# Kernel optimization log

Measured on AMD Instinct MI355X. Metric: run time of the kernel, lower is better.

## Reference

```python
import jax, jax.numpy as jnp
import numpy as np

NEG = -9e15
ALPHA = 0.2  # leaky-relu slope


def gat_layer(h, mask, W, a, concat):
    # h: [N, Fin], W: [Fin, Fout], a: [2*Fout, 1], mask: [N, N]
    Wh = h @ W                                   # [N, Fout]
    F = Wh.shape[1]
    e = jax.nn.leaky_relu(Wh @ a[:F] + (Wh @ a[F:]).T, ALPHA)  # [N, N]
    att = jax.nn.softmax(jnp.where(mask > 0, e, NEG), axis=1)
    out = att @ Wh                               # [N, Fout]
    return jax.nn.elu(out) if concat else out


def gat(x, mask, W, a, Wo, ao):
    # W: [H, Fin, Fhid], a: [H, 2*Fhid, 1]
    heads = jax.vmap(lambda Wi, ai: gat_layer(x, mask, Wi, ai, True))(W, a)  # [H, N, Fhid]
    h = jnp.transpose(heads, (1, 0, 2)).reshape(x.shape[0], -1)  # [N, H*Fhid] (concat dim=1)
    return jax.nn.elu(gat_layer(h, mask, Wo, ao, False))


def setup_inputs() -> dict:
    key = jax.random.key(0)
    ks = jax.random.split(key, 16)
    N, Fin, H, Fhid, Ffin, P = 4096, 256, 4, 64, 64, 16
    x = jax.random.normal(ks[0], (N, Fin), jnp.float32)
    eye = jnp.eye(N, dtype=jnp.float32)
    sadj = jnp.maximum((jax.random.uniform(ks[1], (N, N)) < 0.005).astype(jnp.float32), eye)
    sadj2 = jnp.maximum((jax.random.uniform(ks[2], (N, N)) < 0.005).astype(jnp.float32), eye)
    s = 0.1
    inp = {
        "x": x, "sadj": sadj, "sadj2": sadj2,
        "W1": s * jax.random.normal(ks[3], (H, Fin, Fhid), jnp.float32),
        "a1": s * jax.random.normal(ks[4], (H, 2 * Fhid, 1), jnp.float32),
        "Wo1": s * jax.random.normal(ks[5], (H * Fhid, Ffin), jnp.float32),
        "ao1": s * jax.random.normal(ks[6], (2 * Ffin, 1), jnp.float32),
        "W2": s * jax.random.normal(ks[7], (H, Fin, Fhid), jnp.float32),
        "a2": s * jax.random.normal(ks[8], (H, 2 * Fhid, 1), jnp.float32),
        "Wo2": s * jax.random.normal(ks[9], (H * Fhid, Ffin), jnp.float32),
        "ao2": s * jax.random.normal(ks[10], (2 * Ffin, 1), jnp.float32),
        "Wp1": s * jax.random.normal(ks[11], (Ffin, P), jnp.float32),
        "bp1": jnp.zeros((P,), jnp.float32),
        "Wp2": s * jax.random.normal(ks[12], (P, 1), jnp.float32),
    }
    return inp


def reference(x, sadj, sadj2, W1, a1, Wo1, ao1, W2, a2, Wo2, ao2, Wp1, bp1, Wp2):
    emb1 = gat(x, sadj, W1, a1, Wo1, ao1)    # [N, Ffin]
    emb2 = gat(x, sadj2, W2, a2, Wo2, ao2)   # [N, Ffin]
    emb = jnp.stack([emb1, emb2], axis=1)    # [N, 2, Ffin]
    w = jnp.tanh(emb @ Wp1 + bp1) @ Wp2      # [N, 2, 1]
    beta = jax.nn.softmax(w, axis=1)
    return jnp.sum(beta * emb, axis=1)       # [N, Ffin]
```

## Files before the change

### kernel.cpp

```cpp
#include <hip/hip_runtime.h>
#include <hip/hip_bf16.h>
#include <stdint.h>


typedef short short8 __attribute__((ext_vector_type(8)));
typedef __bf16 bf16x8 __attribute__((ext_vector_type(8)));
typedef float floatx4 __attribute__((ext_vector_type(4)));
typedef unsigned int uintx4 __attribute__((ext_vector_type(4)));

#define MAXDEG 128
#define LRELU 0.2f

template <typename V>
__device__ inline auto mfma_impl(V a, V b, floatx4 c, int)
    -> decltype(__builtin_amdgcn_mfma_f32_16x16x32_bf16(a, b, c, 0, 0, 0)) {
  return __builtin_amdgcn_mfma_f32_16x16x32_bf16(a, b, c, 0, 0, 0);
}
template <typename V>
__device__ inline floatx4 mfma_impl(V a, V b, floatx4 c, long) {
  return __builtin_amdgcn_mfma_f32_16x16x32_bf16(
      __builtin_bit_cast(bf16x8, a), __builtin_bit_cast(bf16x8, b), c, 0, 0, 0);
}
__device__ inline floatx4 MFMA16(short8 a, short8 b, floatx4 c) {
  return mfma_impl(a, b, c, 0);
}

__device__ inline bool is_bf16_inputs(const void* sadj) {
  return ((*(const uint32_t*)sadj) & 0xFFFFu) == 0x3F80u;
}
__device__ inline float ldval(const void* p, size_t i, bool isbf) {
  if (isbf) return __bfloat162float(((const __hip_bfloat16*)p)[i]);
  return ((const float*)p)[i];
}
__device__ inline uint16_t f2bf_bits(float f) {
  __hip_bfloat16 h = __float2bfloat16(f);
  return *(uint16_t*)&h;
}
__device__ inline float bf2f(uint16_t u) {
  uint32_t i = ((uint32_t)u) << 16;
  return __builtin_bit_cast(float, i);
}

static constexpr size_t OFF_ADJ = 0;
static constexpr size_t OFF_DEG = OFF_ADJ + (size_t)2 * 4096 * MAXDEG * 4;
static constexpr size_t OFF_XB  = OFF_DEG + (size_t)2 * 4096 * 4;
static constexpr size_t OFF_WT  = OFF_XB  + (size_t)4096 * 256 * 2;
static constexpr size_t OFF_WOT = OFF_WT  + (size_t)2 * 4 * 64 * 256 * 2;
static constexpr size_t OFF_AV  = OFF_WOT + (size_t)2 * 64 * 256 * 2;
static constexpr size_t OFF_AOV = OFF_AV  + (size_t)2 * 4 * 128 * 4;
static constexpr size_t OFF_WP1 = OFF_AOV + (size_t)2 * 128 * 4;
static constexpr size_t OFF_BP1 = OFF_WP1 + (size_t)64 * 16 * 4;
static constexpr size_t OFF_WP2 = OFF_BP1 + 64;
static constexpr size_t OFF_WH1B = OFF_WP2 + 192;
static constexpr size_t OFF_S1  = OFF_WH1B + (size_t)2 * 4096 * 256 * 2;
static constexpr size_t OFF_D1  = OFF_S1  + (size_t)2 * 4 * 4096 * 4;
static constexpr size_t OFF_H2  = OFF_D1  + (size_t)2 * 4 * 4096 * 4;
static constexpr size_t OFF_WH2B = OFF_H2 + (size_t)2 * 4096 * 256 * 2;
static constexpr size_t OFF_S2  = OFF_WH2B + (size_t)2 * 4096 * 64 * 2;
static constexpr size_t OFF_D2  = OFF_S2  + (size_t)2 * 4096 * 4;
static constexpr size_t OFF_MB  = OFF_D2  + (size_t)2 * 4096 * 4;

__global__ __launch_bounds__(256) void k_pre(const void* sadj, const void* sadj2,
    const void* x,
    const void* W1, const void* W2, const void* Wo1, const void* Wo2,
    const void* a1, const void* a2, const void* ao1, const void* ao2,
    const void* wp1, const void* bp1, const void* wp2,
    uint8_t* mbytes, uint16_t* xb, uint16_t* Wt, uint16_t* Wot,
    float* Av, float* Aov, float* Wp1v, float* Bp1v, float* Wp2v) {
  bool isbf = is_bf16_inputs(sadj);
  int bid = blockIdx.x;
  if (bid < 2048) {
    int tid = bid * 256 + threadIdx.x;
    int nt = 2048 * 256;
    const int NCHUNK = 4194304;
    if (isbf) {
      const uint16_t* m0 = (const uint16_t*)sadj;
      const uint16_t* m1 = (const uint16_t*)sadj2;
      for (int c = tid; c < NCHUNK; c += nt) {
        const uint16_t* src = (c < 2097152) ? m0 : m1;
        int cc = c & 2097151;
        uintx4 v = *((const uintx4*)src + cc);
        uint32_t wd[4] = {v.x, v.y, v.z, v.w};
        uint32_t byte = 0;
#pragma unroll
        for (int k = 0; k < 8; ++k) {
          uint16_t val = (uint16_t)(wd[k >> 1] >> ((k & 1) * 16));
          if (val != 0 && !(val & 0x8000)) byte |= 1u << k;
        }
        mbytes[c] = (uint8_t)byte;
      }
    } else {
      const float* m0 = (const float*)sadj;
      const float* m1 = (const float*)sadj2;
      for (int c = tid; c < NCHUNK; c += nt) {
        const float* src = (c < 2097152) ? m0 : m1;
        size_t cc = (size_t)(c & 2097151) * 8;
        floatx4 va = *(const floatx4*)(src + cc);
        floatx4 vb = *(const floatx4*)(src + cc + 4);
        float vals[8] = {va.x, va.y, va.z, va.w, vb.x, vb.y, vb.z, vb.w};
        uint32_t byte = 0;
#pragma unroll
        for (int k = 0; k < 8; ++k)
          if (vals[k] > 0.f) byte |= 1u << k;
        mbytes[c] = (uint8_t)byte;
      }
    }
    return;
  }
  if (bid < 3072) {
    int i0 = ((bid - 2048) * 256 + threadIdx.x) * 4;
    if (isbf) {
      *(uint64_t*)(xb + i0) = *(const uint64_t*)((const uint16_t*)x + i0);
    } else {
      const float* xf = (const float*)x;
      float4 f = *(const float4*)(xf + i0);
      xb[i0 + 0] = f2bf_bits(f.x);
      xb[i0 + 1] = f2bf_bits(f.y);
      xb[i0 + 2] = f2bf_bits(f.z);
      xb[i0 + 3] = f2bf_bits(f.w);
    }
    return;
  }
  int idx = (bid - 3072) * 256 + threadIdx.x;
  if (idx < 131072) {
    int k = idx & 255, f = (idx >> 8) & 63, h = (idx >> 14) & 3, g = idx >> 16;
    const void* W = g ? W2 : W1;
    Wt[idx] = f2bf_bits(ldval(W, (size_t)h * 16384 + (size_t)k * 64 + f, isbf));
  } else if (idx < 163840) {
    int j = idx - 131072;
    int k = j & 255, f = (j >> 8) & 63, g = j >> 14;
    const void* W = g ? Wo2 : Wo1;
    Wot[j] = f2bf_bits(ldval(W, (size_t)k * 64 + f, isbf));
  } else if (idx < 166176) {
    int q = idx - 163840;
    if (q < 512)        Av[q] = ldval(a1, q, isbf);
    else if (q < 1024)  Av[q] = ldval(a2, q - 512, isbf);
    else if (q < 1152)  Aov[q - 1024] = ldval(ao1, q - 1024, isbf);
    else if (q < 1280)  Aov[q - 1152 + 128] = ldval(ao2, q - 1152, isbf);
    else if (q < 2304)  Wp1v[q - 1280] = ldval(wp1, q - 1280, isbf);
    else if (q < 2320)  Bp1v[q - 2304] = ldval(bp1, q - 2304, isbf);
    else                Wp2v[q - 2320] = ldval(wp2, q - 2320, isbf);
  }
}

__global__ __launch_bounds__(256) void k_cg(const uint8_t* mbytes,
    const uint16_t* xb, const uint16_t* Wt, const float* Av,
    int* adj, int* deg, uint16_t* Wh1b, float* s1, float* d1) {
  int bid = blockIdx.x;
  if (bid < 2048) {
    int w = bid * 4 + (threadIdx.x >> 6);
    int lane = threadIdx.x & 63;
    uint64_t bits = *((const uint64_t*)(mbytes + (size_t)w * 512) + lane);
    int* out = adj + (size_t)w * MAXDEG;
    int c = __popcll(bits);
    int pre = c;
#pragma unroll
    for (int o = 1; o < 64; o <<= 1) {
      int tv = __shfl_up(pre, o);
      if (lane >= o) pre += tv;
    }
    int total = __shfl(pre, 63);
    int off = pre - c;
    int base = lane * 64;
    while (bits) {
      int i = __ffsll((unsigned long long)bits) - 1;
      bits &= bits - 1;
      if (off < MAXDEG) out[off] = base + i;
      ++off;
    }
    if (lane == 0) deg[w] = total < MAXDEG ? total : MAXDEG;
    return;
  }
  int w = (bid - 2048) * 4 + (threadIdx.x >> 6);
  int lane = threadIdx.x & 63;
  int q = lane >> 4, c = lane & 15;
  int g = w >> 10, rem = w & 1023;
  int m0 = (rem >> 2) << 4, h = rem & 3;
  const uint16_t* B = Wt + (size_t)(g * 4 + h) * 64 * 256;
  floatx4 acc[4] = {};
  const uint16_t* arow = xb + (size_t)(m0 + c) * 256 + q * 8;
  for (int kk = 0; kk < 8; ++kk) {
    short8 a = *(const short8*)(arow + kk * 32);
#pragma unroll
    for (int t = 0; t < 4; ++t) {
      short8 b = *(const short8*)(B + (size_t)(t * 16 + c) * 256 + kk * 32 + q * 8);
      acc[t] = MFMA16(a, b, acc[t]);
    }
  }
  uint16_t* Crow = Wh1b + (size_t)(g * 4096 + m0) * 256 + h * 64;
#pragma unroll
  for (int t = 0; t < 4; ++t)
#pragma unroll
    for (int r = 0; r < 4; ++r)
      Crow[(size_t)(q * 4 + r) * 256 + t * 16 + c] = f2bf_bits(acc[t][r]);
  const float* ag = Av + (g * 4 + h) * 128;
  float as[4], ad[4];
#pragma unroll
  for (int t = 0; t < 4; ++t) { as[t] = ag[t * 16 + c]; ad[t] = ag[64 + t * 16 + c]; }
#pragma unroll
  for (int r = 0; r < 4; ++r) {
    float ps = 0.f, pd = 0.f;
#pragma unroll
    for (int t = 0; t < 4; ++t) { ps += acc[t][r] * as[t]; pd += acc[t][r] * ad[t]; }
#pragma unroll
    for (int o = 1; o < 16; o <<= 1) { ps += __shfl_xor(ps, o); pd += __shfl_xor(pd, o); }
    if (c == 0) {
      int n = m0 + q * 4 + r;
      s1[((size_t)(g * 4096 + n)) * 4 + h] = ps;
      d1[((size_t)(g * 4096 + n)) * 4 + h] = pd;
    }
  }
}

__global__ __launch_bounds__(256) void k_att1(const int* adj, const int* deg,
    const float* s1, const float* d1, const uint16_t* Wh1b, uint16_t* h2) {
  __shared__ float pbuf[4][4][MAXDEG];
  __shared__ int jbuf[4][MAXDEG];
  int wv = threadIdx.x >> 6, lane = threadIdx.x & 63;
  int w = blockIdx.x * 4 + wv;
  int g = w >> 12;
  int gn = w;
  int dg = deg[gn];
  const int* nbr = adj + (size_t)gn * MAXDEG;
  float4 s4 = *(const float4*)(s1 + (size_t)gn * 4);
  const float4* d4 = (const float4*)(d1) + (size_t)g * 4096;

  bool v0 = lane < dg, v1 = lane + 64 < dg;
  int j0 = 0, j1 = 0;
  if (v0) j0 = nbr[lane];
  if (v1) j1 = nbr[lane + 64];
  float4 dj0 = d4[j0];
  float4 dj1 = d4[j1];
  if (v0) jbuf[wv][lane] = j0;
  if (v1) jbuf[wv][lane + 64] = j1;

  const float ninf = -3.0e38f;
  float sa[4] = {s4.x, s4.y, s4.z, s4.w};
  float d0a[4] = {dj0.x, dj0.y, dj0.z, dj0.w};
  float d1a[4] = {dj1.x, dj1.y, dj1.z, dj1.w};
#pragma unroll
  for (int h = 0; h < 4; ++h) {
    float t0 = sa[h] + d0a[h]; t0 = t0 > 0.f ? t0 : LRELU * t0;
    float t1 = sa[h] + d1a[h]; t1 = t1 > 0.f ? t1 : LRELU * t1;
    float e0 = v0 ? t0 : ninf;
    float e1 = v1 ? t1 : ninf;
    float m = fmaxf(e0, e1);
#pragma unroll
    for (int o = 32; o; o >>= 1) m = fmaxf(m, __shfl_xor(m, o));
    float p0 = v0 ? __expf(e0 - m) : 0.f;
    float p1 = v1 ? __expf(e1 - m) : 0.f;
    float l = p0 + p1;
#pragma unroll
    for (int o = 32; o; o >>= 1) l += __shfl_xor(l, o);
    float inv = __frcp_rn(l);
    pbuf[wv][h][lane] = p0 * inv;
    pbuf[wv][h][lane + 64] = p1 * inv;
  }
  int myh = lane >> 4;
  const float* prow = pbuf[wv][myh];
  const int* jb = jbuf[wv];
  const uint16_t* Wg = Wh1b + (size_t)g * 4096 * 256;
  float ax = 0.f, ay = 0.f, az = 0.f, aw = 0.f;
  for (int i = 0; i < dg; i += 8) {
    float pv[8];
    ushort4 wv8[8];
#pragma unroll
    for (int k = 0; k < 8; ++k) {
      int idx = i + k;
      bool vv = idx < dg;
      int sidx = vv ? idx : 0;
      int j = jb[sidx];
      pv[k] = vv ? prow[sidx] : 0.f;
      wv8[k] = *(const ushort4*)(Wg + (size_t)j * 256 + lane * 4);
    }
#pragma unroll
    for (int k = 0; k < 8; ++k) {
      ax += pv[k] * bf2f(wv8[k].x);
      ay += pv[k] * bf2f(wv8[k].y);
      az += pv[k] * bf2f(wv8[k].z);
      aw += pv[k] * bf2f(wv8[k].w);
    }
  }
  ax = ax > 0.f ? ax : __expf(ax) - 1.f;
  ay = ay > 0.f ? ay : __expf(ay) - 1.f;
  az = az > 0.f ? az : __expf(az) - 1.f;
  aw = aw > 0.f ? aw : __expf(aw) - 1.f;
  ushort4 o4 = {f2bf_bits(ax), f2bf_bits(ay), f2bf_bits(az), f2bf_bits(aw)};
  *(ushort4*)(h2 + (size_t)gn * 256 + lane * 4) = o4;
}

__global__ __launch_bounds__(256) void k_gemm2(const uint16_t* h2, const uint16_t* Wot,
                                               const float* Aov,
                                               uint16_t* Wh2b, float* s2, float* d2) {
  int w = blockIdx.x * 4 + (threadIdx.x >> 6);
  int lane = threadIdx.x & 63;
  int q = lane >> 4, c = lane & 15;
  int g = w >> 8, m0 = (w & 255) << 4;
  const uint16_t* A = h2 + (size_t)g * 4096 * 256;
  const uint16_t* B = Wot + (size_t)g * 64 * 256;
  floatx4 acc[4] = {};
  const uint16_t* arow = A + (size_t)(m0 + c) * 256 + q * 8;
  for (int kk = 0; kk < 8; ++kk) {
    short8 a = *(const short8*)(arow + kk * 32);
#pragma unroll
    for (int t = 0; t < 4; ++t) {
      short8 b = *(const short8*)(B + (size_t)(t * 16 + c) * 256 + kk * 32 + q * 8);
      acc[t] = MFMA16(a, b, acc[t]);
    }
  }
  uint16_t* Crow = Wh2b + (size_t)(g * 4096 + m0) * 64;
#pragma unroll
  for (int t = 0; t < 4; ++t)
#pragma unroll
    for (int r = 0; r < 4; ++r)
      Crow[(size_t)(q * 4 + r) * 64 + t * 16 + c] = f2bf_bits(acc[t][r]);
  const float* ag = Aov + g * 128;
  float as[4], ad[4];
#pragma unroll
  for (int t = 0; t < 4; ++t) { as[t] = ag[t * 16 + c]; ad[t] = ag[64 + t * 16 + c]; }
#pragma unroll
  for (int r = 0; r < 4; ++r) {
    float ps = 0.f, pd = 0.f;
#pragma unroll
    for (int t = 0; t < 4; ++t) { ps += acc[t][r] * as[t]; pd += acc[t][r] * ad[t]; }
#pragma unroll
    for (int o = 1; o < 16; o <<= 1) { ps += __shfl_xor(ps, o); pd += __shfl_xor(pd, o); }
    if (c == 0) {
      int n = m0 + q * 4 + r;
      s2[g * 4096 + n] = ps;
      d2[g * 4096 + n] = pd;
    }
  }
}

__global__ __launch_bounds__(256) void k_att2f(const int* adj, const int* deg,
    const float* s2, const float* d2, const uint16_t* Wh2b,
    const float* Wp1v, const float* Bp1v, const float* Wp2v,
    const void* sadj, void* out) {
  __shared__ float pbuf[4][MAXDEG];
  __shared__ int jbuf[4][MAXDEG];
  __shared__ float emb_s[4][64];
  __shared__ float st_s[2][32];
  __shared__ float sw_s[2][2];
  int wv = threadIdx.x >> 6, lane = threadIdx.x & 63;
  int g = wv >> 1, nl = wv & 1;
  int n = blockIdx.x * 2 + nl;
  int gn = g * 4096 + n;
  int dg = deg[gn];
  const int* nbr = adj + (size_t)gn * MAXDEG;
  float sn = s2[gn];
  const float* dp = d2 + (size_t)g * 4096;

  bool v0 = lane < dg, v1 = lane + 64 < dg;
  int j0 = 0, j1 = 0;
  if (v0) j0 = nbr[lane];
  if (v1) j1 = nbr[lane + 64];
  float dd0 = dp[j0], dd1 = dp[j1];
  if (v0) jbuf[wv][lane] = j0;
  if (v1) jbuf[wv][lane + 64] = j1;

  const float ninf = -3.0e38f;
  float t0 = sn + dd0; t0 = t0 > 0.f ? t0 : LRELU * t0;
  float t1 = sn + dd1; t1 = t1 > 0.f ? t1 : LRELU * t1;
  float e0 = v0 ? t0 : ninf;
  float e1 = v1 ? t1 : ninf;
  float m = fmaxf(e0, e1);
#pragma unroll
  for (int o = 32; o; o >>= 1) m = fmaxf(m, __shfl_xor(m, o));
  float p0 = v0 ? __expf(e0 - m) : 0.f;
  float p1 = v1 ? __expf(e1 - m) : 0.f;
  float l = p0 + p1;
#pragma unroll
  for (int o = 32; o; o >>= 1) l += __shfl_xor(l, o);
  float inv = __frcp_rn(l);
  pbuf[wv][lane] = p0 * inv;
  pbuf[wv][lane + 64] = p1 * inv;

  int mye = lane >> 4, c4 = lane & 15;
  const uint16_t* Wg = Wh2b + (size_t)g * 4096 * 64;
  float ax = 0.f, ay = 0.f, az = 0.f, aw = 0.f;
  for (int i = 0; i < dg; i += 8) {
    int ia = i + mye, ib = i + 4 + mye;
    bool va = ia < dg, vb = ib < dg;
    int sa_ = va ? ia : 0, sb_ = vb ? ib : 0;
    int ja = jbuf[wv][sa_], jb2 = jbuf[wv][sb_];
    float pa = va ? pbuf[wv][sa_] : 0.f;
    float pb = vb ? pbuf[wv][sb_] : 0.f;
    ushort4 wa = *(const ushort4*)(Wg + (size_t)ja * 64 + c4 * 4);
    ushort4 wb = *(const ushort4*)(Wg + (size_t)jb2 * 64 + c4 * 4);
    ax += pa * bf2f(wa.x) + pb * bf2f(wb.x);
    ay += pa * bf2f(wa.y) + pb * bf2f(wb.y);
    az += pa * bf2f(wa.z) + pb * bf2f(wb.z);
    aw += pa * bf2f(wa.w) + pb * bf2f(wb.w);
  }
#pragma unroll
  for (int o = 16; o <= 32; o <<= 1) {
    ax += __shfl_xor(ax, o);
    ay += __shfl_xor(ay, o);
    az += __shfl_xor(az, o);
    aw += __shfl_xor(aw, o);
  }
  if (lane < 16) {
    ax = ax > 0.f ? ax : __expf(ax) - 1.f;
    ay = ay > 0.f ? ay : __expf(ay) - 1.f;
    az = az > 0.f ? az : __expf(az) - 1.f;
    aw = aw > 0.f ? aw : __expf(aw) - 1.f;
    float4 r = {ax, ay, az, aw};
    *(float4*)&emb_s[wv][c4 * 4] = r;
  }
  __syncthreads();
  if (wv < 2) {
    float e1v = emb_s[wv][lane];
    float e2v = emb_s[2 + wv][lane];
    if (lane < 32) {
      int gg = lane >> 4, p = lane & 15;
      float s = Bp1v[p];
      const float* eb = emb_s[gg * 2 + wv];
      for (int f = 0; f < 64; ++f) s += eb[f] * Wp1v[f * 16 + p];
      st_s[wv][lane] = tanhf(s);
    }
    if (lane < 2) {
      float s = 0.f;
      for (int p = 0; p < 16; ++p) s += st_s[wv][lane * 16 + p] * Wp2v[p];
      sw_s[wv][lane] = s;
    }
    float w0 = sw_s[wv][0], w1 = sw_s[wv][1];
    float mx = fmaxf(w0, w1);
    float q0 = __expf(w0 - mx), q1 = __expf(w1 - mx);
    float qi = 1.f / (q0 + q1);
    float v = (q0 * e1v + q1 * e2v) * qi;
    if (is_bf16_inputs(sadj)) ((uint16_t*)out)[(size_t)n * 64 + lane] = f2bf_bits(v);
    else ((float*)out)[(size_t)n * 64 + lane] = v;
  }
}

extern "C" void kernel_launch(void* const* d_in, const int* in_sizes, int n_in,
                              void* d_out, int out_size, void* d_ws, size_t ws_size,
                              hipStream_t stream) {
  const void* x    = d_in[0];
  const void* sadj = d_in[1];
  const void* sadj2 = d_in[2];
  const void* W1  = d_in[3];
  const void* a1  = d_in[4];
  const void* Wo1 = d_in[5];
  const void* ao1 = d_in[6];
  const void* W2  = d_in[7];
  const void* a2  = d_in[8];
  const void* Wo2 = d_in[9];
  const void* ao2 = d_in[10];
  const void* Wp1 = d_in[11];
  const void* bp1 = d_in[12];
  const void* Wp2 = d_in[13];

  char* ws = (char*)d_ws;
  int* adj      = (int*)(ws + OFF_ADJ);
  int* deg      = (int*)(ws + OFF_DEG);
  uint16_t* xb  = (uint16_t*)(ws + OFF_XB);
  uint16_t* Wt  = (uint16_t*)(ws + OFF_WT);
  uint16_t* Wot = (uint16_t*)(ws + OFF_WOT);
  float* Av     = (float*)(ws + OFF_AV);
  float* Aov    = (float*)(ws + OFF_AOV);
  float* Wp1v   = (float*)(ws + OFF_WP1);
  float* Bp1v   = (float*)(ws + OFF_BP1);
  float* Wp2v   = (float*)(ws + OFF_WP2);
  uint16_t* Wh1b = (uint16_t*)(ws + OFF_WH1B);
  float* s1     = (float*)(ws + OFF_S1);
  float* d1     = (float*)(ws + OFF_D1);
  uint16_t* h2  = (uint16_t*)(ws + OFF_H2);
  uint16_t* Wh2b = (uint16_t*)(ws + OFF_WH2B);
  float* s2     = (float*)(ws + OFF_S2);
  float* d2     = (float*)(ws + OFF_D2);
  uint8_t* mb   = (uint8_t*)(ws + OFF_MB);

  k_pre<<<3728, 256, 0, stream>>>(sadj, sadj2, x, W1, W2, Wo1, Wo2,
                                  a1, a2, ao1, ao2, Wp1, bp1, Wp2,
                                  mb, xb, Wt, Wot, Av, Aov, Wp1v, Bp1v, Wp2v);
  k_cg<<<2560, 256, 0, stream>>>(mb, xb, Wt, Av, adj, deg, Wh1b, s1, d1);
  k_att1<<<2048, 256, 0, stream>>>(adj, deg, s1, d1, Wh1b, h2);
  k_gemm2<<<128, 256, 0, stream>>>(h2, Wot, Aov, Wh2b, s2, d2);
  k_att2f<<<2048, 256, 0, stream>>>(adj, deg, s2, d2, Wh2b,
                                    Wp1v, Bp1v, Wp2v, sadj, d_out);
}
```

Baseline: 232.1 us.

## Build adjacency lists per row directly from masks, dropping packed bitmask stage

Removes the intermediate packed mask-byte buffer. Each adjacency row is now compacted in one 256-thread block that reads the dense mask row, builds bits and does a block-wide prefix scan. The old combined pre/compaction kernel is split into separate adjacency kernels and a standalone first GEMM kernel. A device-to-device copy of the first mask into workspace is also added; it costs extra memory traffic and reserves more workspace, and the copy is only read on the bf16 path.

```diff
diff --git a/kernel.cpp b/kernel.cpp
--- a/kernel.cpp
+++ b/kernel.cpp
@@ -58,57 +58,18 @@
 static constexpr size_t OFF_WH2B = OFF_H2 + (size_t)2 * 4096 * 256 * 2;
 static constexpr size_t OFF_S2  = OFF_WH2B + (size_t)2 * 4096 * 64 * 2;
 static constexpr size_t OFF_D2  = OFF_S2  + (size_t)2 * 4096 * 4;
-static constexpr size_t OFF_MB  = OFF_D2  + (size_t)2 * 4096 * 4;
-
-__global__ __launch_bounds__(256) void k_pre(const void* sadj, const void* sadj2,
-    const void* x,
+static constexpr size_t OFF_M0  = OFF_D2  + (size_t)2 * 4096 * 4;
+
+__global__ __launch_bounds__(256) void k_pre(const void* x,
     const void* W1, const void* W2, const void* Wo1, const void* Wo2,
     const void* a1, const void* a2, const void* ao1, const void* ao2,
-    const void* wp1, const void* bp1, const void* wp2,
-    uint8_t* mbytes, uint16_t* xb, uint16_t* Wt, uint16_t* Wot,
+    const void* wp1, const void* bp1, const void* wp2, const void* sadj,
+    uint16_t* xb, uint16_t* Wt, uint16_t* Wot,
     float* Av, float* Aov, float* Wp1v, float* Bp1v, float* Wp2v) {
   bool isbf = is_bf16_inputs(sadj);
   int bid = blockIdx.x;
-  if (bid < 2048) {
-    int tid = bid * 256 + threadIdx.x;
-    int nt = 2048 * 256;
-    const int NCHUNK = 4194304;
-    if (isbf) {
-      const uint16_t* m0 = (const uint16_t*)sadj;
-      const uint16_t* m1 = (const uint16_t*)sadj2;
-      for (int c = tid; c < NCHUNK; c += nt) {
-        const uint16_t* src = (c < 2097152) ? m0 : m1;
-        int cc = c & 2097151;
-        uintx4 v = *((const uintx4*)src + cc);
-        uint32_t wd[4] = {v.x, v.y, v.z, v.w};
-        uint32_t byte = 0;
-#pragma unroll
-        for (int k = 0; k < 8; ++k) {
-          uint16_t val = (uint16_t)(wd[k >> 1] >> ((k & 1) * 16));
-          if (val != 0 && !(val & 0x8000)) byte |= 1u << k;
-        }
-        mbytes[c] = (uint8_t)byte;
-      }
-    } else {
-      const float* m0 = (const float*)sadj;
-      const float* m1 = (const float*)sadj2;
-      for (int c = tid; c < NCHUNK; c += nt) {
-        const float* src = (c < 2097152) ? m0 : m1;
-        size_t cc = (size_t)(c & 2097151) * 8;
-        floatx4 va = *(const floatx4*)(src + cc);
-        floatx4 vb = *(const floatx4*)(src + cc + 4);
-        float vals[8] = {va.x, va.y, va.z, va.w, vb.x, vb.y, vb.z, vb.w};
-        uint32_t byte = 0;
-#pragma unroll
-        for (int k = 0; k < 8; ++k)
-          if (vals[k] > 0.f) byte |= 1u << k;
-        mbytes[c] = (uint8_t)byte;
-      }
-    }
-    return;
-  }
-  if (bid < 3072) {
-    int i0 = ((bid - 2048) * 256 + threadIdx.x) * 4;
+  if (bid < 1024) {
+    int i0 = (bid * 256 + threadIdx.x) * 4;
     if (isbf) {
       *(uint64_t*)(xb + i0) = *(const uint64_t*)((const uint16_t*)x + i0);
     } else {
@@ -121,7 +82,7 @@
     }
     return;
   }
-  int idx = (bid - 3072) * 256 + threadIdx.x;
+  int idx = (bid - 1024) * 256 + threadIdx.x;
   if (idx < 131072) {
     int k = idx & 255, f = (idx >> 8) & 63, h = (idx >> 14) & 3, g = idx >> 16;
     const void* W = g ? W2 : W1;
@@ -143,35 +104,79 @@
   }
 }
 
-__global__ __launch_bounds__(256) void k_cg(const uint8_t* mbytes,
-    const uint16_t* xb, const uint16_t* Wt, const float* Av,
-    int* adj, int* deg, uint16_t* Wh1b, float* s1, float* d1) {
-  int bid = blockIdx.x;
-  if (bid < 2048) {
-    int w = bid * 4 + (threadIdx.x >> 6);
-    int lane = threadIdx.x & 63;
-    uint64_t bits = *((const uint64_t*)(mbytes + (size_t)w * 512) + lane);
-    int* out = adj + (size_t)w * MAXDEG;
-    int c = __popcll(bits);
-    int pre = c;
-#pragma unroll
-    for (int o = 1; o < 64; o <<= 1) {
-      int tv = __shfl_up(pre, o);
-      if (lane >= o) pre += tv;
-    }
-    int total = __shfl(pre, 63);
-    int off = pre - c;
-    int base = lane * 64;
-    while (bits) {
-      int i = __ffsll((unsigned long long)bits) - 1;
-      bits &= bits - 1;
-      if (off < MAXDEG) out[off] = base + i;
-      ++off;
-    }
-    if (lane == 0) deg[w] = total < MAXDEG ? total : MAXDEG;
-    return;
-  }
-  int w = (bid - 2048) * 4 + (threadIdx.x >> 6);
+__device__ inline void adj_row(const uint16_t* mrow_bf, const float* mrow_f32,
+                               bool isbf, int gn, int* adj, int* deg) {
+  __shared__ int wtot[4];
+  int t = threadIdx.x;
+  uint32_t bits = 0;
+  if (isbf) {
+    uintx4 v0 = *((const uintx4*)mrow_bf + 2 * t);
+    uintx4 v1 = *((const uintx4*)mrow_bf + 2 * t + 1);
+    uint32_t wd[8] = {v0.x, v0.y, v0.z, v0.w, v1.x, v1.y, v1.z, v1.w};
+#pragma unroll
+    for (int k = 0; k < 16; ++k) {
+      uint16_t val = (uint16_t)(wd[k >> 1] >> ((k & 1) * 16));
+      if (val != 0 && !(val & 0x8000)) bits |= 1u << k;
+    }
+  } else {
+#pragma unroll
+    for (int j = 0; j < 4; ++j) {
+      floatx4 v = *((const floatx4*)mrow_f32 + 4 * t + j);
+      if (v.x > 0.f) bits |= 1u << (4 * j + 0);
+      if (v.y > 0.f) bits |= 1u << (4 * j + 1);
+      if (v.z > 0.f) bits |= 1u << (4 * j + 2);
+      if (v.w > 0.f) bits |= 1u << (4 * j + 3);
+    }
+  }
+  int c = __popc(bits);
+  int lane = t & 63, wid = t >> 6;
+  int pre = c;
+#pragma unroll
+  for (int o = 1; o < 64; o <<= 1) {
+    int tv = __shfl_up(pre, o);
+    if (lane >= o) pre += tv;
+  }
+  if (lane == 63) wtot[wid] = pre;
+  __syncthreads();
+  int base = 0, total = 0;
+#pragma unroll
+  for (int wq = 0; wq < 4; ++wq) {
+    int v = wtot[wq];
+    if (wq < wid) base += v;
+    total += v;
+  }
+  int off = base + pre - c;
+  int colbase = t * 16;
+  int* out = adj + (size_t)gn * MAXDEG;
+  while (bits) {
+    int i = __ffs(bits) - 1;
+    bits &= bits - 1;
+    if (off < MAXDEG) out[off] = colbase + i;
+    ++off;
+  }
+  if (t == 0) deg[gn] = total < MAXDEG ? total : MAXDEG;
+}
+
+__global__ __launch_bounds__(256) void k_adjA(const uint16_t* m0ws, const void* sadj,
+                                              int* adj, int* deg) {
+  bool isbf = is_bf16_inputs(sadj);
+  int row = blockIdx.x;
+  adj_row(m0ws + (size_t)row * 4096,
+          (const float*)sadj + (size_t)row * 4096, isbf, row, adj, deg);
+}
+
+__global__ __launch_bounds__(256) void k_adjB(const void* sadj2,
+                                              int* adj, int* deg) {
+  bool isbf = is_bf16_inputs(sadj2);
+  int row = blockIdx.x;
+  adj_row((const uint16_t*)sadj2 + (size_t)row * 4096,
+          (const float*)sadj2 + (size_t)row * 4096, isbf, 4096 + row, adj, deg);
+}
+
+__global__ __launch_bounds__(256) void k_gemm1(const uint16_t* xb, const uint16_t* Wt,
+                                               const float* Av,
+                                               uint16_t* Wh1b, float* s1, float* d1) {
+  int w = blockIdx.x * 4 + (threadIdx.x >> 6);
   int lane = threadIdx.x & 63;
   int q = lane >> 4, c = lane & 15;
   int g = w >> 10, rem = w & 1023;
@@ -470,12 +475,16 @@
   uint16_t* Wh2b = (uint16_t*)(ws + OFF_WH2B);
   float* s2     = (float*)(ws + OFF_S2);
   float* d2     = (float*)(ws + OFF_D2);
-  uint8_t* mb   = (uint8_t*)(ws + OFF_MB);
-
-  k_pre<<<3728, 256, 0, stream>>>(sadj, sadj2, x, W1, W2, Wo1, Wo2,
-                                  a1, a2, ao1, ao2, Wp1, bp1, Wp2,
-                                  mb, xb, Wt, Wot, Av, Aov, Wp1v, Bp1v, Wp2v);
-  k_cg<<<2560, 256, 0, stream>>>(mb, xb, Wt, Av, adj, deg, Wh1b, s1, d1);
+  uint16_t* m0  = (uint16_t*)(ws + OFF_M0);
+
+  hipMemcpyAsync(m0, sadj, (size_t)4096 * 4096 * 2, hipMemcpyDeviceToDevice,
+                 stream);
+  k_pre<<<1680, 256, 0, stream>>>(x, W1, W2, Wo1, Wo2, a1, a2, ao1, ao2,
+                                  Wp1, bp1, Wp2, sadj,
+                                  xb, Wt, Wot, Av, Aov, Wp1v, Bp1v, Wp2v);
+  k_adjA<<<4096, 256, 0, stream>>>(m0, sadj, adj, deg);
+  k_adjB<<<4096, 256, 0, stream>>>(sadj2, adj, deg);
+  k_gemm1<<<512, 256, 0, stream>>>(xb, Wt, Av, Wh1b, s1, d1);
   k_att1<<<2048, 256, 0, stream>>>(adj, deg, s1, d1, Wh1b, h2);
   k_gemm2<<<128, 256, 0, stream>>>(h2, Wot, Aov, Wh2b, s2, d2);
   k_att2f<<<2048, 256, 0, stream>>>(adj, deg, s2, d2, Wh2b,
```

After: 235.2 us. About the same (+1.3%).
